# Performance work log

Measured on AMD Instinct MI355X. Metric: run time of the kernel, lower is better.

The kernel has to match this reference:

```python
import jax, jax.numpy as jnp
import numpy as np

GAMMA = 0.99
LAMDA = 0.95
EPS = 1e-8
T = 16777216  # number of steps


def setup_inputs() -> dict:
    key = jax.random.key(0)
    k1, k2, k3 = jax.random.split(key, 3)
    rewards = jax.random.normal(k1, (T,), dtype=jnp.float32)
    v_pred = jax.random.normal(k2, (T + 1,), dtype=jnp.float32)
    dones = jax.random.randint(k3, (T,), 0, 2, dtype=jnp.int32)
    return {"rewards": rewards, "v_pred": v_pred, "dones": dones}


def reference(rewards, v_pred, dones):
    not_done = 1.0 - dones.astype(rewards.dtype)  # [T]
    # TD residual with reset at done: delta_k = r_k + gamma*V_{k+1}*(1-done_k) - V_k
    delta = rewards + GAMMA * v_pred[1:] * not_done - v_pred[:-1]
    # continuation coefficient: adv_k = delta_k + gamma*lamda*(1-done_k)*adv_{k+1}
    cont = (GAMMA * LAMDA) * not_done

    def step(carry, xs):
        d, c = xs
        a = d + c * carry
        return a, a

    _, adv = jax.lax.scan(step, jnp.zeros((), rewards.dtype), (delta, cont), reverse=True)
    # standardize (stateless): (x - mean) / (std + eps)
    adv = (adv - jnp.mean(adv)) / (jnp.std(adv) + EPS)
    return adv
```

## Files before the change

kernel.cpp:

```cpp
#include <hip/hip_runtime.h>


#define GAMMA_F 0.99f
#define GL_F 0.9405f
#define EPS_F 1e-8f

constexpr int NT = 256;
constexpr int PL = 8;
constexpr int TILE = 512;
constexpr int CHUNK = 2 * TILE;
constexpr int K2T = 1024;

__device__ __forceinline__ void tile_scan(const float4& r0, const float4& r1,
                                          const float4& v0, const float4& v1,
                                          const float* nd, float vn63, int lane,
                                          float* d, float* c,
                                          float& sD, float& sC, float& S1D, float& S1C) {
    float vnext = __shfl_down(v0.x, 1);
    if (lane == 63) vnext = vn63;
    float va[9] = {v0.x, v0.y, v0.z, v0.w, v1.x, v1.y, v1.z, v1.w, vnext};
    float rf[8] = {r0.x, r0.y, r0.z, r0.w, r1.x, r1.y, r1.z, r1.w};
#pragma unroll
    for (int i = 0; i < 8; ++i) {
        d[i] = rf[i] + GAMMA_F * va[i + 1] * nd[i] - va[i];
        c[i] = GL_F * nd[i];
    }
    float D = 0.f, C = 1.f;
#pragma unroll
    for (int i = 7; i >= 0; --i) { D = d[i] + c[i] * D; C *= c[i]; }
#pragma unroll
    for (int off = 1; off < 64; off <<= 1) {
        float tD = __shfl_down(D, off);
        float tC = __shfl_down(C, off);
        if (lane + off < 64) { D = D + C * tD; C = C * tC; }
    }
    sD = D; sC = C;
    S1D = __shfl_down(D, 1); S1C = __shfl_down(C, 1);
    if (lane == 63) { S1D = 0.f; S1C = 1.f; }
}

__device__ __forceinline__ void lane_moms(const float* d, const float* c,
                                          float S1D, float S1C, float* mm) {
    float x = S1D, P = S1C;
    float A = 0.f, Pp = 0.f, L2 = 0.f, LP = 0.f, P2 = 0.f;
#pragma unroll
    for (int i = 7; i >= 0; --i) {
        x = d[i] + c[i] * x;
        P *= c[i];
        A += x; Pp += P; L2 += x * x; LP += x * P; P2 += P * P;
    }
    mm[0] = A; mm[1] = Pp; mm[2] = L2; mm[3] = LP; mm[4] = P2;
}

__global__ __launch_bounds__(NT) void k_desc(const float* __restrict__ r,
                                             const float* __restrict__ v,
                                             const int* __restrict__ dn,
                                             float2* __restrict__ desc,
                                             float4* __restrict__ mom4,
                                             float* __restrict__ mom1,
                                             unsigned long long* __restrict__ dmask) {
    const int tid = threadIdx.x, lane = tid & 63, wv = tid >> 6;
    const int ch = blockIdx.x * 4 + wv;
    const int base = ch * CHUNK;
    const int o0 = base + lane * PL, o1 = base + TILE + lane * PL;

    float4 r00 = *(const float4*)(r + o0), r01 = *(const float4*)(r + o0 + 4);
    float4 v00 = *(const float4*)(v + o0), v01 = *(const float4*)(v + o0 + 4);
    int4   a00 = *(const int4*)(dn + o0),  a01 = *(const int4*)(dn + o0 + 4);
    float4 r10 = *(const float4*)(r + o1), r11 = *(const float4*)(r + o1 + 4);
    float4 v10 = *(const float4*)(v + o1), v11 = *(const float4*)(v + o1 + 4);
    int4   a10 = *(const int4*)(dn + o1),  a11 = *(const int4*)(dn + o1 + 4);

    float vn63_t1 = (lane == 63) ? v[base + CHUNK] : 0.f;
    float vn63_t0 = __shfl(v10.x, 0);

    int di0[8] = {a00.x, a00.y, a00.z, a00.w, a01.x, a01.y, a01.z, a01.w};
    int di1[8] = {a10.x, a10.y, a10.z, a10.w, a11.x, a11.y, a11.z, a11.w};
    float nd0[8], nd1[8];
    unsigned long long m0[8], m1[8];
#pragma unroll
    for (int i = 0; i < 8; ++i) {
        nd0[i] = 1.f - (float)di0[i]; m0[i] = __ballot(di0[i] != 0);
        nd1[i] = 1.f - (float)di1[i]; m1[i] = __ballot(di1[i] != 0);
    }

    float d1[8], c1[8], sD1, sC1, S1D1, S1C1;
    tile_scan(r10, r11, v10, v11, nd1, vn63_t1, lane, d1, c1, sD1, sC1, S1D1, S1C1);
    const float T1D = __shfl(sD1, 0), T1C = __shfl(sC1, 0);
    float d0[8], c0[8], sD0, sC0, S1D0, S1C0;
    tile_scan(r00, r01, v00, v01, nd0, vn63_t0, lane, d0, c0, sD0, sC0, S1D0, S1C0);
    const float T0D = __shfl(sD0, 0), T0C = __shfl(sC0, 0);

    float mm1[5], mm0[5];
    lane_moms(d1, c1, S1D1, S1C1, mm1);
    lane_moms(d0, c0, S1D0, S1C0, mm0);
    const float e = T1D, f = T1C;
    float gA  = mm1[0] + mm0[0] + e * mm0[1];
    float gP  = mm1[1] + f * mm0[1];
    float gL2 = mm1[2] + mm0[2] + 2.f * e * mm0[3] + e * e * mm0[4];
    float gLP = mm1[3] + f * (mm0[3] + e * mm0[4]);
    float gP2 = mm1[4] + f * f * mm0[4];
#pragma unroll
    for (int off = 32; off > 0; off >>= 1) {
        gA  += __shfl_down(gA,  off);
        gP  += __shfl_down(gP,  off);
        gL2 += __shfl_down(gL2, off);
        gLP += __shfl_down(gLP, off);
        gP2 += __shfl_down(gP2, off);
    }
    if (lane == 0) {
        desc[ch] = make_float2(T0D + T0C * T1D, T0C * T1C);
        mom4[ch] = make_float4(gA, gP, gL2, gLP);
        mom1[ch] = gP2;
        unsigned long long* mp = dmask + (size_t)ch * 16;
#pragma unroll
        for (int i = 0; i < 8; ++i) { mp[i] = m0[i]; mp[8 + i] = m1[i]; }
    }
}

__global__ __launch_bounds__(K2T) void k_scan(const float2* __restrict__ desc,
                                              const float4* __restrict__ mom4,
                                              const float* __restrict__ mom1,
                                              float* __restrict__ carry,
                                              float2* __restrict__ meanstd,
                                              int nchunk, long long T) {
    const int t = threadIdx.x;
    const int per = nchunk / K2T;
    const int s = t * per;
    float D = 0.f, C = 1.f;
    for (int i = per - 1; i >= 0; --i) { float2 a = desc[s + i]; D = a.x + a.y * D; C *= a.y; }
    __shared__ float Ds[K2T], Cs[K2T];
    Ds[t] = D; Cs[t] = C;
    __syncthreads();
    for (int off = 1; off < K2T; off <<= 1) {
        float d2 = 0.f, c2 = 0.f;
        bool act = (t + off) < K2T;
        if (act) { d2 = Ds[t + off]; c2 = Cs[t + off]; }
        __syncthreads();
        if (act) { float a = Ds[t] + Cs[t] * d2; float b = Cs[t] * c2; Ds[t] = a; Cs[t] = b; }
        __syncthreads();
    }
    float x = (t + 1 < K2T) ? Ds[t + 1] : 0.f;
    double gS = 0.0, gQ = 0.0;
    for (int i = per - 1; i >= 0; --i) {
        const int cix = s + i;
        carry[cix] = x;
        float4 m = mom4[cix];
        float p2 = mom1[cix];
        gS += (double)(m.x + x * m.y);
        gQ += (double)(m.z + 2.f * x * m.w + x * x * p2);
        float2 a = desc[cix];
        x = a.x + a.y * x;
    }
    for (int off = 32; off > 0; off >>= 1) {
        gS += __shfl_down(gS, off);
        gQ += __shfl_down(gQ, off);
    }
    __shared__ double Sa[K2T / 64], Sb[K2T / 64];
    const int wv = t >> 6, lane = t & 63;
    if (lane == 0) { Sa[wv] = gS; Sb[wv] = gQ; }
    __syncthreads();
    if (t == 0) {
        double S = 0.0, Q = 0.0;
        for (int w = 0; w < K2T / 64; ++w) { S += Sa[w]; Q += Sb[w]; }
        double mean = S / (double)T;
        double var = Q / (double)T - mean * mean;
        double sd = sqrt(var > 0.0 ? var : 0.0);
        meanstd[0] = make_float2((float)mean, (float)(1.0 / (sd + (double)EPS_F)));
    }
}

__global__ __launch_bounds__(NT) void k_apply(const float* __restrict__ r,
                                              const float* __restrict__ v,
                                              const unsigned long long* __restrict__ dmask,
                                              const float* __restrict__ carry,
                                              const float2* __restrict__ meanstd,
                                              float* __restrict__ out) {
    const int tid = threadIdx.x, lane = tid & 63, wv = tid >> 6;
    const int ch = blockIdx.x * 4 + wv;
    const int base = ch * CHUNK;
    const int o0 = base + lane * PL, o1 = base + TILE + lane * PL;

    float4 r00 = *(const float4*)(r + o0), r01 = *(const float4*)(r + o0 + 4);
    float4 v00 = *(const float4*)(v + o0), v01 = *(const float4*)(v + o0 + 4);
    float4 r10 = *(const float4*)(r + o1), r11 = *(const float4*)(r + o1 + 4);
    float4 v10 = *(const float4*)(v + o1), v11 = *(const float4*)(v + o1 + 4);
    const unsigned long long* mp = dmask + (size_t)ch * 16;

    float vn63_t1 = (lane == 63) ? v[base + CHUNK] : 0.f;
    float vn63_t0 = __shfl(v10.x, 0);
    const float2 ms = meanstd[0];
    const float cy = carry[ch];

    float nd0[8], nd1[8];
#pragma unroll
    for (int i = 0; i < 8; ++i) {
        nd0[i] = 1.f - (float)((mp[i] >> lane) & 1ull);
        nd1[i] = 1.f - (float)((mp[8 + i] >> lane) & 1ull);
    }

    float d1[8], c1[8], sD1, sC1, S1D1, S1C1;
    tile_scan(r10, r11, v10, v11, nd1, vn63_t1, lane, d1, c1, sD1, sC1, S1D1, S1C1);
    const float T1D = __shfl(sD1, 0), T1C = __shfl(sC1, 0);
    float d0[8], c0[8], sD0, sC0, S1D0, S1C0;
    tile_scan(r00, r01, v00, v01, nd0, vn63_t0, lane, d0, c0, sD0, sC0, S1D0, S1C0);

    float o[8];
    float x = S1D1 + S1C1 * cy;
#pragma unroll
    for (int i = 7; i >= 0; --i) { x = d1[i] + c1[i] * x; o[i] = (x - ms.x) * ms.y; }
    *(float4*)(out + o1)     = make_float4(o[0], o[1], o[2], o[3]);
    *(float4*)(out + o1 + 4) = make_float4(o[4], o[5], o[6], o[7]);
    const float x0e = T1D + T1C * cy;
    x = S1D0 + S1C0 * x0e;
#pragma unroll
    for (int i = 7; i >= 0; --i) { x = d0[i] + c0[i] * x; o[i] = (x - ms.x) * ms.y; }
    *(float4*)(out + o0)     = make_float4(o[0], o[1], o[2], o[3]);
    *(float4*)(out + o0 + 4) = make_float4(o[4], o[5], o[6], o[7]);
}

extern "C" void kernel_launch(void* const* d_in, const int* in_sizes, int n_in,
                              void* d_out, int out_size, void* d_ws, size_t ws_size,
                              hipStream_t stream) {
    const float* rewards = (const float*)d_in[0];
    const float* v_pred  = (const float*)d_in[1];
    const int*   dones   = (const int*)d_in[2];
    float* out = (float*)d_out;
    const long long T = in_sizes[0];
    const int nchunk = (int)(T / CHUNK);

    char* ws = (char*)d_ws;
    float4* mom4 = (float4*)ws;
    size_t off = (size_t)nchunk * 16;
    float2* desc = (float2*)(ws + off);  off += (size_t)nchunk * 8;
    float*  mom1 = (float*)(ws + off);   off += (size_t)nchunk * 4;
    float*  carry = (float*)(ws + off);  off += (size_t)nchunk * 4;
    float2* meanstd = (float2*)(ws + off); off += 16;
    unsigned long long* dmask = (unsigned long long*)(ws + off);

    hipLaunchKernelGGL(k_desc, dim3(nchunk / 4), dim3(NT), 0, stream,
                       rewards, v_pred, dones, desc, mom4, mom1, dmask);
    hipLaunchKernelGGL(k_scan, dim3(1), dim3(K2T), 0, stream,
                       desc, mom4, mom1, carry, meanstd, nchunk, T);
    hipLaunchKernelGGL(k_apply, dim3(nchunk / 4), dim3(NT), 0, stream,
                       rewards, v_pred, dmask, carry, meanstd, out);
}
```

Before: 115.8 us.

## Store fp16 TD residuals in first pass and apply scan from them

```diff
diff --git a/kernel.cpp b/kernel.cpp
--- a/kernel.cpp
+++ b/kernel.cpp
@@ -1,4 +1,5 @@
 #include <hip/hip_runtime.h>
+#include <hip/hip_fp16.h>
 
 
 #define GAMMA_F 0.99f
@@ -6,50 +7,83 @@
 #define EPS_F 1e-8f
 
 constexpr int NT = 256;
-constexpr int PL = 8;
-constexpr int TILE = 512;
-constexpr int CHUNK = 2 * TILE;
+constexpr int TILE = 256;
+constexpr int TPC = 4;
+constexpr int CHUNK = TILE * TPC;
 constexpr int K2T = 1024;
 
-__device__ __forceinline__ void tile_scan(const float4& r0, const float4& r1,
-                                          const float4& v0, const float4& v1,
-                                          const float* nd, float vn63, int lane,
-                                          float* d, float* c,
-                                          float& sD, float& sC, float& S1D, float& S1C) {
-    float vnext = __shfl_down(v0.x, 1);
-    if (lane == 63) vnext = vn63;
-    float va[9] = {v0.x, v0.y, v0.z, v0.w, v1.x, v1.y, v1.z, v1.w, vnext};
-    float rf[8] = {r0.x, r0.y, r0.z, r0.w, r1.x, r1.y, r1.z, r1.w};
-#pragma unroll
-    for (int i = 0; i < 8; ++i) {
-        d[i] = rf[i] + GAMMA_F * va[i + 1] * nd[i] - va[i];
-        c[i] = GL_F * nd[i];
-    }
+union H4 { __half h[4]; uint2 u2; };
+
+struct TR { float4 rr, vv; int4 dd; float vx; };
+
+__device__ __forceinline__ void load_tile(const float* __restrict__ r,
+                                          const float* __restrict__ v,
+                                          const int* __restrict__ dn,
+                                          int tb, int lane, TR& t) {
+    const int e = tb + lane * 4;
+    t.rr = *(const float4*)(r + e);
+    t.vv = *(const float4*)(v + e);
+    t.dd = *(const int4*)(dn + e);
+    t.vx = 0.f;
+    if (lane == 63) t.vx = v[tb + TILE];
+}
+
+__device__ __forceinline__ void process_tile(const TR& tr, int lane, int ch, int t,
+                                             __half* __restrict__ dh,
+                                             unsigned long long* __restrict__ dmask,
+                                             int tb,
+                                             float& KD, float& KC,
+                                             float& gA, float& gP, float& gL2,
+                                             float& gLP, float& gP2) {
+    float vnext = __shfl_down(tr.vv.x, 1);
+    if (lane == 63) vnext = tr.vx;
+    float va[5] = {tr.vv.x, tr.vv.y, tr.vv.z, tr.vv.w, vnext};
+    float rf[4] = {tr.rr.x, tr.rr.y, tr.rr.z, tr.rr.w};
+    int   di[4] = {tr.dd.x, tr.dd.y, tr.dd.z, tr.dd.w};
+    float d[4], c[4];
+    unsigned long long mb[4];
+#pragma unroll
+    for (int i = 0; i < 4; ++i) {
+        float nd = 1.f - (float)di[i];
+        d[i] = rf[i] + GAMMA_F * va[i + 1] * nd - va[i];
+        c[i] = GL_F * nd;
+        mb[i] = __ballot(di[i] != 0);
+    }
+    H4 u;
+#pragma unroll
+    for (int i = 0; i < 4; ++i) u.h[i] = __float2half(d[i]);
+    *(uint2*)(dh + tb + lane * 4) = u.u2;
+    unsigned long long mv = mb[0];
+    if (lane == 1) mv = mb[1];
+    if (lane == 2) mv = mb[2];
+    if (lane == 3) mv = mb[3];
+    if (lane < 4) dmask[(size_t)ch * 16 + t * 4 + lane] = mv;
     float D = 0.f, C = 1.f;
 #pragma unroll
-    for (int i = 7; i >= 0; --i) { D = d[i] + c[i] * D; C *= c[i]; }
+    for (int i = 3; i >= 0; --i) { D = d[i] + c[i] * D; C *= c[i]; }
 #pragma unroll
     for (int off = 1; off < 64; off <<= 1) {
-        float tD = __shfl_down(D, off);
-        float tC = __shfl_down(C, off);
+        float tD = __shfl_down(D, off), tC = __shfl_down(C, off);
         if (lane + off < 64) { D = D + C * tD; C = C * tC; }
     }
-    sD = D; sC = C;
-    S1D = __shfl_down(D, 1); S1C = __shfl_down(C, 1);
+    float S1D = __shfl_down(D, 1), S1C = __shfl_down(C, 1);
     if (lane == 63) { S1D = 0.f; S1C = 1.f; }
-}
-
-__device__ __forceinline__ void lane_moms(const float* d, const float* c,
-                                          float S1D, float S1C, float* mm) {
-    float x = S1D, P = S1C;
-    float A = 0.f, Pp = 0.f, L2 = 0.f, LP = 0.f, P2 = 0.f;
-#pragma unroll
-    for (int i = 7; i >= 0; --i) {
-        x = d[i] + c[i] * x;
-        P *= c[i];
+    const float tD0 = __shfl(D, 0), tC0 = __shfl(C, 0);
+    float x = S1D, P = S1C, A = 0.f, Pp = 0.f, L2 = 0.f, LP = 0.f, P2 = 0.f;
+#pragma unroll
+    for (int i = 3; i >= 0; --i) {
+        x = d[i] + c[i] * x; P *= c[i];
         A += x; Pp += P; L2 += x * x; LP += x * P; P2 += P * P;
     }
-    mm[0] = A; mm[1] = Pp; mm[2] = L2; mm[3] = LP; mm[4] = P2;
+    const float e = tD0, f = tC0;
+    float nA  = gA + e * gP + A;
+    float nL2 = gL2 + 2.f * e * gLP + e * e * gP2 + L2;
+    float nLP = f * (gLP + e * gP2) + LP;
+    float nP2 = f * f * gP2 + P2;
+    float nP  = f * gP + Pp;
+    gA = nA; gL2 = nL2; gLP = nLP; gP2 = nP2; gP = nP;
+    float nKD = KD + KC * tD0;
+    KC = KC * tC0; KD = nKD;
 }
 
 __global__ __launch_bounds__(NT) void k_desc(const float* __restrict__ r,
@@ -58,48 +92,21 @@
                                              float2* __restrict__ desc,
                                              float4* __restrict__ mom4,
                                              float* __restrict__ mom1,
-                                             unsigned long long* __restrict__ dmask) {
+                                             unsigned long long* __restrict__ dmask,
+                                             __half* __restrict__ dh) {
     const int tid = threadIdx.x, lane = tid & 63, wv = tid >> 6;
     const int ch = blockIdx.x * 4 + wv;
     const int base = ch * CHUNK;
-    const int o0 = base + lane * PL, o1 = base + TILE + lane * PL;
-
-    float4 r00 = *(const float4*)(r + o0), r01 = *(const float4*)(r + o0 + 4);
-    float4 v00 = *(const float4*)(v + o0), v01 = *(const float4*)(v + o0 + 4);
-    int4   a00 = *(const int4*)(dn + o0),  a01 = *(const int4*)(dn + o0 + 4);
-    float4 r10 = *(const float4*)(r + o1), r11 = *(const float4*)(r + o1 + 4);
-    float4 v10 = *(const float4*)(v + o1), v11 = *(const float4*)(v + o1 + 4);
-    int4   a10 = *(const int4*)(dn + o1),  a11 = *(const int4*)(dn + o1 + 4);
-
-    float vn63_t1 = (lane == 63) ? v[base + CHUNK] : 0.f;
-    float vn63_t0 = __shfl(v10.x, 0);
-
-    int di0[8] = {a00.x, a00.y, a00.z, a00.w, a01.x, a01.y, a01.z, a01.w};
-    int di1[8] = {a10.x, a10.y, a10.z, a10.w, a11.x, a11.y, a11.z, a11.w};
-    float nd0[8], nd1[8];
-    unsigned long long m0[8], m1[8];
-#pragma unroll
-    for (int i = 0; i < 8; ++i) {
-        nd0[i] = 1.f - (float)di0[i]; m0[i] = __ballot(di0[i] != 0);
-        nd1[i] = 1.f - (float)di1[i]; m1[i] = __ballot(di1[i] != 0);
-    }
-
-    float d1[8], c1[8], sD1, sC1, S1D1, S1C1;
-    tile_scan(r10, r11, v10, v11, nd1, vn63_t1, lane, d1, c1, sD1, sC1, S1D1, S1C1);
-    const float T1D = __shfl(sD1, 0), T1C = __shfl(sC1, 0);
-    float d0[8], c0[8], sD0, sC0, S1D0, S1C0;
-    tile_scan(r00, r01, v00, v01, nd0, vn63_t0, lane, d0, c0, sD0, sC0, S1D0, S1C0);
-    const float T0D = __shfl(sD0, 0), T0C = __shfl(sC0, 0);
-
-    float mm1[5], mm0[5];
-    lane_moms(d1, c1, S1D1, S1C1, mm1);
-    lane_moms(d0, c0, S1D0, S1C0, mm0);
-    const float e = T1D, f = T1C;
-    float gA  = mm1[0] + mm0[0] + e * mm0[1];
-    float gP  = mm1[1] + f * mm0[1];
-    float gL2 = mm1[2] + mm0[2] + 2.f * e * mm0[3] + e * e * mm0[4];
-    float gLP = mm1[3] + f * (mm0[3] + e * mm0[4]);
-    float gP2 = mm1[4] + f * f * mm0[4];
+    float KD = 0.f, KC = 1.f, gA = 0.f, gP = 0.f, gL2 = 0.f, gLP = 0.f, gP2 = 0.f;
+    TR ta, tb;
+    load_tile(r, v, dn, base + 0 * TILE, lane, ta);
+    load_tile(r, v, dn, base + 1 * TILE, lane, tb);
+    process_tile(ta, lane, ch, 0, dh, dmask, base + 0 * TILE, KD, KC, gA, gP, gL2, gLP, gP2);
+    load_tile(r, v, dn, base + 2 * TILE, lane, ta);
+    process_tile(tb, lane, ch, 1, dh, dmask, base + 1 * TILE, KD, KC, gA, gP, gL2, gLP, gP2);
+    load_tile(r, v, dn, base + 3 * TILE, lane, tb);
+    process_tile(ta, lane, ch, 2, dh, dmask, base + 2 * TILE, KD, KC, gA, gP, gL2, gLP, gP2);
+    process_tile(tb, lane, ch, 3, dh, dmask, base + 3 * TILE, KD, KC, gA, gP, gL2, gLP, gP2);
 #pragma unroll
     for (int off = 32; off > 0; off >>= 1) {
         gA  += __shfl_down(gA,  off);
@@ -109,12 +116,9 @@
         gP2 += __shfl_down(gP2, off);
     }
     if (lane == 0) {
-        desc[ch] = make_float2(T0D + T0C * T1D, T0C * T1C);
+        desc[ch] = make_float2(KD, KC);
         mom4[ch] = make_float4(gA, gP, gL2, gLP);
         mom1[ch] = gP2;
-        unsigned long long* mp = dmask + (size_t)ch * 16;
-#pragma unroll
-        for (int i = 0; i < 8; ++i) { mp[i] = m0[i]; mp[8 + i] = m1[i]; }
     }
 }
 
@@ -124,23 +128,25 @@
                                               float* __restrict__ carry,
                                               float2* __restrict__ meanstd,
                                               int nchunk, long long T) {
-    const int t = threadIdx.x;
+    const int t = threadIdx.x, lane = t & 63, wv = t >> 6;
     const int per = nchunk / K2T;
     const int s = t * per;
     float D = 0.f, C = 1.f;
     for (int i = per - 1; i >= 0; --i) { float2 a = desc[s + i]; D = a.x + a.y * D; C *= a.y; }
-    __shared__ float Ds[K2T], Cs[K2T];
-    Ds[t] = D; Cs[t] = C;
+    float sD = D, sC = C;
+#pragma unroll
+    for (int off = 1; off < 64; off <<= 1) {
+        float tD = __shfl_down(sD, off), tC = __shfl_down(sC, off);
+        if (lane + off < 64) { sD = sD + sC * tD; sC = sC * tC; }
+    }
+    __shared__ float2 waff[16];
+    if (lane == 0) waff[wv] = make_float2(sD, sC);
     __syncthreads();
-    for (int off = 1; off < K2T; off <<= 1) {
-        float d2 = 0.f, c2 = 0.f;
-        bool act = (t + off) < K2T;
-        if (act) { d2 = Ds[t + off]; c2 = Cs[t + off]; }
-        __syncthreads();
-        if (act) { float a = Ds[t] + Cs[t] * d2; float b = Cs[t] * c2; Ds[t] = a; Cs[t] = b; }
-        __syncthreads();
-    }
-    float x = (t + 1 < K2T) ? Ds[t + 1] : 0.f;
+    float xw = 0.f;
+    for (int w = 15; w > wv; --w) xw = waff[w].x + waff[w].y * xw;
+    float S1D = __shfl_down(sD, 1), S1C = __shfl_down(sC, 1);
+    if (lane == 63) { S1D = 0.f; S1C = 1.f; }
+    float x = S1D + S1C * xw;
     double gS = 0.0, gQ = 0.0;
     for (int i = per - 1; i >= 0; --i) {
         const int cix = s + i;
@@ -152,17 +158,17 @@
         float2 a = desc[cix];
         x = a.x + a.y * x;
     }
+#pragma unroll
     for (int off = 32; off > 0; off >>= 1) {
         gS += __shfl_down(gS, off);
         gQ += __shfl_down(gQ, off);
     }
-    __shared__ double Sa[K2T / 64], Sb[K2T / 64];
-    const int wv = t >> 6, lane = t & 63;
+    __shared__ double Sa[16], Sb[16];
     if (lane == 0) { Sa[wv] = gS; Sb[wv] = gQ; }
     __syncthreads();
     if (t == 0) {
         double S = 0.0, Q = 0.0;
-        for (int w = 0; w < K2T / 64; ++w) { S += Sa[w]; Q += Sb[w]; }
+        for (int w = 0; w < 16; ++w) { S += Sa[w]; Q += Sb[w]; }
         double mean = S / (double)T;
         double var = Q / (double)T - mean * mean;
         double sd = sqrt(var > 0.0 ? var : 0.0);
@@ -170,8 +176,7 @@
     }
 }
 
-__global__ __launch_bounds__(NT) void k_apply(const float* __restrict__ r,
-                                              const float* __restrict__ v,
+__global__ __launch_bounds__(NT) void k_apply(const __half* __restrict__ dh,
                                               const unsigned long long* __restrict__ dmask,
                                               const float* __restrict__ carry,
                                               const float2* __restrict__ meanstd,
@@ -179,44 +184,38 @@
     const int tid = threadIdx.x, lane = tid & 63, wv = tid >> 6;
     const int ch = blockIdx.x * 4 + wv;
     const int base = ch * CHUNK;
-    const int o0 = base + lane * PL, o1 = base + TILE + lane * PL;
-
-    float4 r00 = *(const float4*)(r + o0), r01 = *(const float4*)(r + o0 + 4);
-    float4 v00 = *(const float4*)(v + o0), v01 = *(const float4*)(v + o0 + 4);
-    float4 r10 = *(const float4*)(r + o1), r11 = *(const float4*)(r + o1 + 4);
-    float4 v10 = *(const float4*)(v + o1), v11 = *(const float4*)(v + o1 + 4);
+    H4 u[4];
+#pragma unroll
+    for (int t = 0; t < 4; ++t) u[t].u2 = *(const uint2*)(dh + base + t * TILE + lane * 4);
     const unsigned long long* mp = dmask + (size_t)ch * 16;
-
-    float vn63_t1 = (lane == 63) ? v[base + CHUNK] : 0.f;
-    float vn63_t0 = __shfl(v10.x, 0);
-    const float2 ms = meanstd[0];
-    const float cy = carry[ch];
-
-    float nd0[8], nd1[8];
-#pragma unroll
-    for (int i = 0; i < 8; ++i) {
-        nd0[i] = 1.f - (float)((mp[i] >> lane) & 1ull);
-        nd1[i] = 1.f - (float)((mp[8 + i] >> lane) & 1ull);
-    }
-
-    float d1[8], c1[8], sD1, sC1, S1D1, S1C1;
-    tile_scan(r10, r11, v10, v11, nd1, vn63_t1, lane, d1, c1, sD1, sC1, S1D1, S1C1);
-    const float T1D = __shfl(sD1, 0), T1C = __shfl(sC1, 0);
-    float d0[8], c0[8], sD0, sC0, S1D0, S1C0;
-    tile_scan(r00, r01, v00, v01, nd0, vn63_t0, lane, d0, c0, sD0, sC0, S1D0, S1C0);
-
-    float o[8];
-    float x = S1D1 + S1C1 * cy;
-#pragma unroll
-    for (int i = 7; i >= 0; --i) { x = d1[i] + c1[i] * x; o[i] = (x - ms.x) * ms.y; }
-    *(float4*)(out + o1)     = make_float4(o[0], o[1], o[2], o[3]);
-    *(float4*)(out + o1 + 4) = make_float4(o[4], o[5], o[6], o[7]);
-    const float x0e = T1D + T1C * cy;
-    x = S1D0 + S1C0 * x0e;
-#pragma unroll
-    for (int i = 7; i >= 0; --i) { x = d0[i] + c0[i] * x; o[i] = (x - ms.x) * ms.y; }
-    *(float4*)(out + o0)     = make_float4(o[0], o[1], o[2], o[3]);
-    *(float4*)(out + o0 + 4) = make_float4(o[4], o[5], o[6], o[7]);
+    const float2 ms = *meanstd;
+    float x = carry[ch];
+#pragma unroll
+    for (int t = 3; t >= 0; --t) {
+        float d[4], c[4];
+#pragma unroll
+        for (int i = 0; i < 4; ++i) {
+            d[i] = __half2float(u[t].h[i]);
+            c[i] = GL_F * (1.f - (float)((mp[t * 4 + i] >> lane) & 1ull));
+        }
+        float D = 0.f, C = 1.f;
+#pragma unroll
+        for (int i = 3; i >= 0; --i) { D = d[i] + c[i] * D; C *= c[i]; }
+#pragma unroll
+        for (int off = 1; off < 64; off <<= 1) {
+            float tD = __shfl_down(D, off), tC = __shfl_down(C, off);
+            if (lane + off < 64) { D = D + C * tD; C = C * tC; }
+        }
+        float S1D = __shfl_down(D, 1), S1C = __shfl_down(C, 1);
+        if (lane == 63) { S1D = 0.f; S1C = 1.f; }
+        const float tD0 = __shfl(D, 0), tC0 = __shfl(C, 0);
+        float xi = S1D + S1C * x;
+        float o[4];
+#pragma unroll
+        for (int i = 3; i >= 0; --i) { xi = d[i] + c[i] * xi; o[i] = (xi - ms.x) * ms.y; }
+        *(float4*)(out + base + t * TILE + lane * 4) = make_float4(o[0], o[1], o[2], o[3]);
+        x = tD0 + tC0 * x;
+    }
 }
 
 extern "C" void kernel_launch(void* const* d_in, const int* in_sizes, int n_in,
@@ -231,17 +230,18 @@
 
     char* ws = (char*)d_ws;
     float4* mom4 = (float4*)ws;
-    size_t off = (size_t)nchunk * 16;
-    float2* desc = (float2*)(ws + off);  off += (size_t)nchunk * 8;
-    float*  mom1 = (float*)(ws + off);   off += (size_t)nchunk * 4;
-    float*  carry = (float*)(ws + off);  off += (size_t)nchunk * 4;
-    float2* meanstd = (float2*)(ws + off); off += 16;
-    unsigned long long* dmask = (unsigned long long*)(ws + off);
+    float2* desc = (float2*)(ws + (size_t)nchunk * 16);
+    float*  mom1 = (float*)(ws + (size_t)nchunk * 24);
+    float*  carry = (float*)(ws + (size_t)nchunk * 28);
+    float2* meanstd = (float2*)(ws + (size_t)nchunk * 32);
+    unsigned long long* dmask =
+        (unsigned long long*)(ws + (size_t)nchunk * 32 + 16);
+    __half* dh = (__half*)(ws + 4ull * 1024 * 1024);
 
     hipLaunchKernelGGL(k_desc, dim3(nchunk / 4), dim3(NT), 0, stream,
-                       rewards, v_pred, dones, desc, mom4, mom1, dmask);
+                       rewards, v_pred, dones, desc, mom4, mom1, dmask, dh);
     hipLaunchKernelGGL(k_scan, dim3(1), dim3(K2T), 0, stream,
                        desc, mom4, mom1, carry, meanstd, nchunk, T);
     hipLaunchKernelGGL(k_apply, dim3(nchunk / 4), dim3(NT), 0, stream,
-                       rewards, v_pred, dmask, carry, meanstd, out);
-}
+                       dh, dmask, carry, meanstd, out);
+}
```

Result: slower. 122.5 us (+5.8%).
